# Kernel optimization log

Hardware: AMD Instinct MI355X
Metric: run time of the kernel (lower is better)

Reference implementation:

```python
import jax, jax.numpy as jnp
import numpy as np

SENSOR_DIM = 256
MODEL_DIM = 512
NUM_DATASETS = 8


def setup_inputs() -> dict:
    key = jax.random.key(0)
    k1, k2, k3 = jax.random.split(key, 3)
    x = jax.random.normal(k1, (32, 200, 1024), dtype=jnp.float32)
    dataset_id = jax.random.randint(k2, (32,), 0, NUM_DATASETS)
    # Conv1d weight [out_ch, in_ch, k] and bias, as in torch.nn.Conv1d
    W = jax.random.normal(k3, (NUM_DATASETS * MODEL_DIM, SENSOR_DIM, 3), dtype=jnp.float32) * 0.02
    b = jnp.zeros((NUM_DATASETS * MODEL_DIM,), dtype=jnp.float32)
    return {"x": x, "dataset_id": dataset_id, "W": W, "b": b}


def reference(x, dataset_id, W, b):
    B, c_in, T = x.shape
    # DatasetPadding: zero-pad channel dim up to sensor_dim
    if c_in < SENSOR_DIM:
        x = jnp.pad(x, ((0, 0), (0, SENSOR_DIM - c_in), (0, 0)))
    # Conv1d(sensor_dim -> num_datasets*model_dim, kernel=3, padding=1)
    y = jax.lax.conv_general_dilated(
        x, W, window_strides=(1,), padding=((1, 1),),
        dimension_numbers=("NCH", "OIH", "NCH"))
    y = y + b[None, :, None]
    y = jax.nn.gelu(y, approximate=False)  # torch GELU default = exact erf
    # unflatten channels to (num_datasets, model_dim) and select per-example dataset slice
    y = y.reshape(B, NUM_DATASETS, MODEL_DIM, T)
    onehot = jax.nn.one_hot(dataset_id, NUM_DATASETS, dtype=y.dtype)  # [B, D]
    out = jnp.einsum("bdmt,bd->bmt", y, onehot)  # [B, model_dim, T]
    return out
```

## Files before the change

### kernel.cpp

```cpp
#include <hip/hip_runtime.h>


typedef unsigned short u16;
typedef __attribute__((ext_vector_type(8))) short bf16x8;
typedef __attribute__((ext_vector_type(4))) float f32x4;

#define CIN 200
#define CINP 224
#define T 1024
#define BATCH 32
#define MD 512
#define XT_ROWS 1026
#define NCHUNK 7
#define XP_PITCH 202
#define TT 256
#define XROWS (TT + 2)
#define XGRAN (XROWS * 4)
#define WOB 256
#define WF_PER_OB (21 * 512)

__device__ __forceinline__ u16 f2bf(float f) {
    unsigned u = __float_as_uint(f);
    u += 0x7FFFu + ((u >> 16) & 1u);
    return (u16)(u >> 16);
}

__device__ __forceinline__ void g2l16(void* lds, const void* g) {
    __builtin_amdgcn_global_load_lds(
        (const __attribute__((address_space(1))) unsigned int*)(uintptr_t)g,
        (__attribute__((address_space(3))) unsigned int*)(unsigned)(uintptr_t)lds,
        16, 0, 0);
}

__global__ __launch_bounds__(256) void prep(const float* __restrict__ x,
                                            const float* __restrict__ W,
                                            u16* __restrict__ xt,
                                            u16* __restrict__ wf) {
    __shared__ __align__(16) unsigned char smem[16 * 673 * 4];
    const int tid = threadIdx.x;
    if (blockIdx.x < 512) {
        u16* tile = (u16*)smem;
        const int b  = blockIdx.x >> 4;
        const int bx = blockIdx.x & 15;
        const int t0 = bx * 64;
        const int tl = tid & 63;
        const int w  = tid >> 6;
        const float* xb = x + (size_t)b * CIN * T + t0 + tl;
        for (int i = w; i < CIN; i += 4)
            tile[tl * XP_PITCH + i] = f2bf(xb[(size_t)i * T]);
        __syncthreads();
        u16* xrow = xt + ((size_t)b * XT_ROWS + 1 + t0) * CINP;
        for (int it = 0; it < 16; ++it) {
            int r = it * 4 + w;
            if (tl < 56) {
                ushort4 v = {0, 0, 0, 0};
                if (tl < 50) {
                    const u16* p = tile + r * XP_PITCH + tl * 4;
                    v.x = p[0]; v.y = p[1]; v.z = p[2]; v.w = p[3];
                }
                *(ushort4*)(xrow + (size_t)r * CINP + tl * 4) = v;
            }
        }
        if (bx == 0 && tid < 112)
            ((unsigned*)(xt + (size_t)b * XT_ROWS * CINP))[tid] = 0;
        if (bx == 15 && tid < 112)
            ((unsigned*)(xt + ((size_t)b * XT_ROWS + 1025) * CINP))[tid] = 0;
    } else {
        float* wtile = (float*)smem;
        const int ob = blockIdx.x - 512;
        const float* wp = W + (size_t)ob * 16 * 768;
        for (int j = tid; j < 16 * 672; j += 256) {
            int o = j / 672, r = j - o * 672;
            wtile[o * 673 + r] = wp[(size_t)o * 768 + r];
        }
        __syncthreads();
        u16* wo = wf + (size_t)ob * WF_PER_OB;
        for (int j = tid; j < WF_PER_OB; j += 256) {
            int e    = j & 7;
            int lane = (j >> 3) & 63;
            int kc   = j >> 9;
            int cc   = kc % 7, k = kc / 7;
            int l = lane & 15, q = lane >> 4;
            int i = cc * 32 + q * 8 + e;
            wo[j] = f2bf(wtile[l * 673 + i * 3 + k]);
        }
    }
}

__global__ __launch_bounds__(256, 2) void conv_mfma(const u16* __restrict__ xt,
                                                    const u16* __restrict__ wf,
                                                    const int* __restrict__ dsid,
                                                    const float* __restrict__ bias,
                                                    float* __restrict__ out) {
    __shared__ __align__(16) u16 xs[2 * XGRAN * 8];

    const int tid = threadIdx.x;
    const int wave = tid >> 6, lane = tid & 63;
    const int l = lane & 15, quad = lane >> 4;
    const int wm  = (wave & 1) * 64;
    const int wti = (wave >> 1) * 128;

    const int id = blockIdx.x;
    const int tb = (id >> 5) * 8 + (id & 7);
    const int m0 = ((id >> 3) & 3) * 128;
    const int t0 = (tb & 3) * TT;
    const int b  = tb >> 2;
    const int d  = dsid[b];
    const int obase = d * MD + m0;

    f32x4 acc[4][8];
#pragma unroll
    for (int mi = 0; mi < 4; ++mi)
#pragma unroll
        for (int ti = 0; ti < 8; ++ti) acc[mi][ti] = (f32x4){0.f, 0.f, 0.f, 0.f};

    const u16* xbase = xt + ((size_t)b * XT_ROWS + t0) * CINP;
    const u16* wfw = wf + (size_t)((obase + wm) >> 4) * WF_PER_OB + lane * 8;

    const u16* xsrc[5]; u16* xdst[5];
#pragma unroll
    for (int k = 0; k < 5; ++k) {
        int g = tid + k * 256;
        int r = g >> 2, p = g & 3, s = p ^ ((r >> 1) & 3);
        if (g < XGRAN) { xsrc[k] = xbase + (size_t)r * CINP + s * 8; xdst[k] = xs + (size_t)(g & ~63) * 8; }
        else           { xsrc[k] = xbase;                            xdst[k] = xs; }
    }

    auto stage = [&](int bsel, int c) {
        const int ic  = c * 32;
        const int off = bsel * (XGRAN * 8);
#pragma unroll
        for (int k = 0; k < 5; ++k)
            if (tid + k * 256 < XGRAN) g2l16(xdst[k] + off, xsrc[k] + ic);
    };
    auto loadw = [&](bf16x8* dst, int tap, int c) {
#pragma unroll
        for (int mi = 0; mi < 4; ++mi)
            dst[mi] = *(const bf16x8*)(wfw + (size_t)((mi * 21 + tap * 7 + c) << 9));
    };

    bf16x8 acur[4], anxt[4];
    stage(0, 0);
    loadw(acur, 0, 0);
    __syncthreads();

#pragma unroll
    for (int c = 0; c < NCHUNK; ++c) {
        const int bsel = c & 1;
        const u16* xb = xs + bsel * (XGRAN * 8);
#pragma unroll
        for (int tap = 0; tap < 3; ++tap) {
            if (tap == 2 && c + 1 < NCHUNK) stage(bsel ^ 1, c + 1);
            if (!(tap == 2 && c == NCHUNK - 1))
                loadw(anxt, (tap == 2 ? 0 : tap + 1), (tap == 2 ? c + 1 : c));
#pragma unroll
            for (int ti = 0; ti < 8; ++ti) {
                int row = wti + tap + ti * 16 + l;
                bf16x8 bv = *(const bf16x8*)(xb + ((size_t)row * 4 + (quad ^ ((row >> 1) & 3))) * 8);
                __builtin_amdgcn_s_setprio(1);
#pragma unroll
                for (int mi = 0; mi < 4; ++mi)
                    acc[mi][ti] = __builtin_amdgcn_mfma_f32_16x16x32_bf16(acur[mi], bv, acc[mi][ti], 0, 0, 0);
                __builtin_amdgcn_s_setprio(0);
            }
#pragma unroll
            for (int mi = 0; mi < 4; ++mi) acur[mi] = anxt[mi];
        }
        if (c + 1 < NCHUNK) __syncthreads();
    }

#pragma unroll
    for (int mi = 0; mi < 4; ++mi) {
        float bvv[4];
#pragma unroll
        for (int r = 0; r < 4; ++r)
            bvv[r] = bias[obase + wm + mi * 16 + quad * 4 + r];
#pragma unroll
        for (int ti = 0; ti < 8; ++ti) {
            int t = t0 + wti + ti * 16 + l;
#pragma unroll
            for (int r = 0; r < 4; ++r) {
                int m = wm + mi * 16 + quad * 4 + r;
                float v = acc[mi][ti][r] + bvv[r];
                float p2 = v * v;
                float z2 = v * fmaf(p2, -0.10295089f, -2.30243665f);
                float e = __builtin_amdgcn_exp2f(z2);
                float g = v * __builtin_amdgcn_rcpf(1.0f + e);
                out[((size_t)(b * MD + m0 + m)) * T + t] = g;
            }
        }
    }
}

extern "C" void kernel_launch(void* const* d_in, const int* in_sizes, int n_in,
                              void* d_out, int out_size, void* d_ws, size_t ws_size,
                              hipStream_t stream) {
    const float* x    = (const float*)d_in[0];
    const int*   dsid = (const int*)d_in[1];
    const float* W    = (const float*)d_in[2];
    const float* bias = (const float*)d_in[3];
    float* out = (float*)d_out;

    u16* xt = (u16*)d_ws;
    u16* wf = xt + (size_t)BATCH * XT_ROWS * CINP;

    prep<<<512 + WOB, 256, 0, stream>>>(x, W, xt, wf);
    conv_mfma<<<512, 256, 0, stream>>>(xt, wf, dsid, bias, out);
}
```

Before: 124.0 us.

## Halve time tile, raise occupancy, stage epilogue through LDS for coalesced stores

Shrinks the per-block time tile from 256 to 128, doubling the grid to 1024 blocks and halving the accumulators so three blocks per CU can be resident. The epilogue now writes GELU results into an LDS buffer in four passes and then stores rows as contiguous float2 vectors, replacing the strided per-element global writes. The next chunk's x prefetch is issued earlier, at tap 0 instead of tap 2. The cost is that each block reuses its weight fragments over fewer time columns, and the epilogue adds extra barriers.

```diff
diff --git a/kernel.cpp b/kernel.cpp
--- a/kernel.cpp
+++ b/kernel.cpp
@@ -13,9 +13,10 @@
 #define XT_ROWS 1026
 #define NCHUNK 7
 #define XP_PITCH 202
-#define TT 256
+#define TT 128
 #define XROWS (TT + 2)
 #define XGRAN (XROWS * 4)
+#define EP_PITCH 130
 #define WOB 256
 #define WF_PER_OB (21 * 512)
 
@@ -87,7 +88,7 @@
     }
 }
 
-__global__ __launch_bounds__(256, 2) void conv_mfma(const u16* __restrict__ xt,
+__global__ __launch_bounds__(256, 3) void conv_mfma(const u16* __restrict__ xt,
                                                     const u16* __restrict__ wf,
                                                     const int* __restrict__ dsid,
                                                     const float* __restrict__ bias,
@@ -98,28 +99,28 @@
     const int wave = tid >> 6, lane = tid & 63;
     const int l = lane & 15, quad = lane >> 4;
     const int wm  = (wave & 1) * 64;
-    const int wti = (wave >> 1) * 128;
+    const int wti = (wave >> 1) * 64;
 
     const int id = blockIdx.x;
     const int tb = (id >> 5) * 8 + (id & 7);
     const int m0 = ((id >> 3) & 3) * 128;
-    const int t0 = (tb & 3) * TT;
-    const int b  = tb >> 2;
+    const int t0 = (tb & 7) * TT;
+    const int b  = tb >> 3;
     const int d  = dsid[b];
     const int obase = d * MD + m0;
 
-    f32x4 acc[4][8];
+    f32x4 acc[4][4];
 #pragma unroll
     for (int mi = 0; mi < 4; ++mi)
 #pragma unroll
-        for (int ti = 0; ti < 8; ++ti) acc[mi][ti] = (f32x4){0.f, 0.f, 0.f, 0.f};
+        for (int ti = 0; ti < 4; ++ti) acc[mi][ti] = (f32x4){0.f, 0.f, 0.f, 0.f};
 
     const u16* xbase = xt + ((size_t)b * XT_ROWS + t0) * CINP;
     const u16* wfw = wf + (size_t)((obase + wm) >> 4) * WF_PER_OB + lane * 8;
 
-    const u16* xsrc[5]; u16* xdst[5];
-#pragma unroll
-    for (int k = 0; k < 5; ++k) {
+    const u16* xsrc[3]; u16* xdst[3];
+#pragma unroll
+    for (int k = 0; k < 3; ++k) {
         int g = tid + k * 256;
         int r = g >> 2, p = g & 3, s = p ^ ((r >> 1) & 3);
         if (g < XGRAN) { xsrc[k] = xbase + (size_t)r * CINP + s * 8; xdst[k] = xs + (size_t)(g & ~63) * 8; }
@@ -130,7 +131,7 @@
         const int ic  = c * 32;
         const int off = bsel * (XGRAN * 8);
 #pragma unroll
-        for (int k = 0; k < 5; ++k)
+        for (int k = 0; k < 3; ++k)
             if (tid + k * 256 < XGRAN) g2l16(xdst[k] + off, xsrc[k] + ic);
     };
     auto loadw = [&](bf16x8* dst, int tap, int c) {
@@ -150,11 +151,11 @@
         const u16* xb = xs + bsel * (XGRAN * 8);
 #pragma unroll
         for (int tap = 0; tap < 3; ++tap) {
-            if (tap == 2 && c + 1 < NCHUNK) stage(bsel ^ 1, c + 1);
             if (!(tap == 2 && c == NCHUNK - 1))
                 loadw(anxt, (tap == 2 ? 0 : tap + 1), (tap == 2 ? c + 1 : c));
-#pragma unroll
-            for (int ti = 0; ti < 8; ++ti) {
+            if (tap == 0 && c + 1 < NCHUNK) stage(bsel ^ 1, c + 1);
+#pragma unroll
+            for (int ti = 0; ti < 4; ++ti) {
                 int row = wti + tap + ti * 16 + l;
                 bf16x8 bv = *(const bf16x8*)(xb + ((size_t)row * 4 + (quad ^ ((row >> 1) & 3))) * 8);
                 __builtin_amdgcn_s_setprio(1);
@@ -169,25 +170,42 @@
         if (c + 1 < NCHUNK) __syncthreads();
     }
 
-#pragma unroll
-    for (int mi = 0; mi < 4; ++mi) {
-        float bvv[4];
+    float bvv[4][4];
+#pragma unroll
+    for (int mi = 0; mi < 4; ++mi)
 #pragma unroll
         for (int r = 0; r < 4; ++r)
-            bvv[r] = bias[obase + wm + mi * 16 + quad * 4 + r];
-#pragma unroll
-        for (int ti = 0; ti < 8; ++ti) {
-            int t = t0 + wti + ti * 16 + l;
-#pragma unroll
-            for (int r = 0; r < 4; ++r) {
-                int m = wm + mi * 16 + quad * 4 + r;
-                float v = acc[mi][ti][r] + bvv[r];
-                float p2 = v * v;
-                float z2 = v * fmaf(p2, -0.10295089f, -2.30243665f);
-                float e = __builtin_amdgcn_exp2f(z2);
-                float g = v * __builtin_amdgcn_rcpf(1.0f + e);
-                out[((size_t)(b * MD + m0 + m)) * T + t] = g;
+            bvv[mi][r] = bias[obase + wm + mi * 16 + quad * 4 + r];
+
+    float* ep = (float*)xs;
+    const int myhalf = wave & 1;
+#pragma unroll
+    for (int p = 0; p < 4; ++p) {
+        __syncthreads();
+        if ((p >> 1) == myhalf) {
+#pragma unroll
+            for (int j = 0; j < 2; ++j) {
+                int mi = 2 * (p & 1) + j;
+#pragma unroll
+                for (int ti = 0; ti < 4; ++ti) {
+#pragma unroll
+                    for (int r = 0; r < 4; ++r) {
+                        float v = acc[mi][ti][r] + bvv[mi][r];
+                        float p2 = v * v;
+                        float z2 = v * fmaf(p2, -0.10295089f, -2.30243665f);
+                        float e = __builtin_amdgcn_exp2f(z2);
+                        float g = v * __builtin_amdgcn_rcpf(1.0f + e);
+                        ep[(j * 16 + quad * 4 + r) * EP_PITCH + wti + ti * 16 + l] = g;
+                    }
+                }
             }
+        }
+        __syncthreads();
+#pragma unroll
+        for (int rr = 0; rr < 8; ++rr) {
+            int row = wave * 8 + rr;
+            float2 v = *(const float2*)(ep + row * EP_PITCH + lane * 2);
+            *(float2*)(out + ((size_t)(b * MD + m0 + p * 32 + row)) * T + t0 + lane * 2) = v;
         }
     }
 }
@@ -205,5 +223,5 @@
     u16* wf = xt + (size_t)BATCH * XT_ROWS * CINP;
 
     prep<<<512 + WOB, 256, 0, stream>>>(x, W, xt, wf);
-    conv_mfma<<<512, 256, 0, stream>>>(xt, wf, dsid, bias, out);
-}
+    conv_mfma<<<1024, 256, 0, stream>>>(xt, wf, dsid, bias, out);
+}
```

After: 133.3 us. 1.08x slower.
